# Optimization experiments

Measured on AMD Instinct MI355X. Metric: run time of the kernel, lower is better.

The kernel has to match this reference:

```python
import jax, jax.numpy as jnp
import numpy as np

B, S, HID = 2, 2048, 2048
H, KVH, D = 16, 4, 128
GROUPS = H // KVH  # 4


def apply_rotary(x, cos, sin):
    # x: [B, h, S, D]; cos/sin: [S, D//2]
    xr = x[..., 0::2]
    xi = x[..., 1::2]
    c = cos[None, None, :, :]
    s = sin[None, None, :, :]
    orr = xr * c - xi * s
    oi = xr * s + xi * c
    return jnp.stack([orr, oi], axis=-1).reshape(x.shape)


def setup_inputs() -> dict:
    key = jax.random.key(0)
    k0, k1, k2, k3, k4 = jax.random.split(key, 5)
    x = jax.random.normal(k0, (B, S, HID), dtype=jnp.float32)
    # real RoPE frequencies (llama-style), stored as [S, D//2, 2] = (cos, sin)
    inv_freq = 1.0 / (10000.0 ** (np.arange(0, D, 2, dtype=np.float32) / D))
    t = np.arange(S, dtype=np.float32)
    ang = np.outer(t, inv_freq)  # [S, D//2]
    freqs_cis = jnp.asarray(np.stack([np.cos(ang), np.sin(ang)], axis=-1), dtype=jnp.float32)
    sc = 0.02
    wq = jax.random.normal(k1, (HID, H * D), dtype=jnp.float32) * sc
    wk = jax.random.normal(k2, (HID, KVH * D), dtype=jnp.float32) * sc
    wv = jax.random.normal(k3, (HID, KVH * D), dtype=jnp.float32) * sc
    wo = jax.random.normal(k4, (H * D, HID), dtype=jnp.float32) * sc
    return {"x": x, "freqs_cis": freqs_cis, "wq": wq, "wk": wk, "wv": wv, "wo": wo}


def reference(x, freqs_cis, wq, wk, wv, wo):
    b, s, _ = x.shape
    cos, sin = freqs_cis[..., 0], freqs_cis[..., 1]
    q = (x @ wq).reshape(b, s, H, D).transpose(0, 2, 1, 3)    # [B,H,S,D]
    k = (x @ wk).reshape(b, s, KVH, D).transpose(0, 2, 1, 3)  # [B,KVH,S,D]
    v = (x @ wv).reshape(b, s, KVH, D).transpose(0, 2, 1, 3)
    q = apply_rotary(q, cos, sin)
    k = apply_rotary(k, cos, sin)
    # GQA expand: repeat kv heads into query-head groups
    k = jnp.repeat(k, GROUPS, axis=1)  # [B,H,S,D]
    v = jnp.repeat(v, GROUPS, axis=1)
    scale = 1.0 / jnp.sqrt(jnp.asarray(D, dtype=x.dtype))
    scores = jnp.einsum("bhqd,bhkd->bhqk", q, k) * scale
    causal = jnp.tril(jnp.ones((s, s), dtype=bool))
    scores = jnp.where(causal[None, None], scores, jnp.asarray(-jnp.inf, dtype=scores.dtype))
    attn = jax.nn.softmax(scores, axis=-1)
    out = jnp.einsum("bhqk,bhkd->bhqd", attn, v)
    out = out.transpose(0, 2, 1, 3).reshape(b, s, H * D)
    return out @ wo
```

## Files before the change

### kernel.cpp

```cpp
#include <hip/hip_runtime.h>
#include <hip/hip_bf16.h>

#define B_   2
#define S_   2048
#define HID_ 2048
#define H_   16
#define KVH_ 4
#define D_   128
#define M_   4096
#define NQKV 3072

typedef __attribute__((ext_vector_type(8))) short bf16x8;
typedef __attribute__((ext_vector_type(4))) float f32x4;
typedef __attribute__((ext_vector_type(16))) float f32x16;
typedef const __attribute__((address_space(1))) unsigned int* gas_p;
typedef __attribute__((address_space(3))) unsigned int* las_p;

__device__ __forceinline__ unsigned short f2b(float f) {
    __hip_bfloat16 h = __float2bfloat16(f);
    return *reinterpret_cast<unsigned short*>(&h);
}
__device__ __forceinline__ float b2f(unsigned short u) {
    __hip_bfloat16 h;
    *reinterpret_cast<unsigned short*>(&h) = u;
    return __bfloat162float(h);
}

__global__ __launch_bounds__(256)
void convert_x(const float* __restrict__ x, unsigned short* __restrict__ xb) {
    int i = (blockIdx.x * 256 + threadIdx.x) * 4;
    float4 v = *(const float4*)(x + i);
    ushort4 o;
    o.x = f2b(v.x); o.y = f2b(v.y); o.z = f2b(v.z); o.w = f2b(v.w);
    *(ushort4*)(xb + i) = o;
}

__global__ __launch_bounds__(256)
void convert_w_all(const float* __restrict__ wq, const float* __restrict__ wk,
                   const float* __restrict__ wv, const float* __restrict__ wo,
                   unsigned short* __restrict__ wqkvT,
                   unsigned short* __restrict__ woT) {
    __shared__ float tile[32][33];
    int z = blockIdx.z;
    const float* w; int N, nbase; unsigned short* dst;
    if (z == 0)      { w = wq; N = 2048; nbase = 0;    dst = wqkvT; }
    else if (z == 1) { w = wk; N = 512;  nbase = 2048; dst = wqkvT; }
    else if (z == 2) { w = wv; N = 512;  nbase = 2560; dst = wqkvT; }
    else             { w = wo; N = 2048; nbase = 0;    dst = woT; }
    int n0 = blockIdx.x * 32, k0 = blockIdx.y * 32;
    if (n0 >= N) return;
    int tx = threadIdx.x & 31, ty = threadIdx.x >> 5;
    #pragma unroll
    for (int j = 0; j < 4; j++)
        tile[ty + j*8][tx] = w[(size_t)(k0 + ty + j*8) * N + n0 + tx];
    __syncthreads();
    #pragma unroll
    for (int j = 0; j < 4; j++)
        dst[(size_t)(nbase + n0 + ty + j*8) * 2048 + k0 + tx] = f2b(tile[tx][ty + j*8]);
}

#define BAR    asm volatile("s_barrier" ::: "memory")
#define LG0    do { asm volatile("s_waitcnt lgkmcnt(0)" ::: "memory"); \
                    __builtin_amdgcn_sched_barrier(0); } while (0)
#define GATE6  asm volatile("s_waitcnt vmcnt(6)" ::: "memory")
#define GATE0  asm volatile("s_waitcnt vmcnt(0)" ::: "memory")
#define PHI    __builtin_amdgcn_s_setprio(1)
#define PLO    __builtin_amdgcn_s_setprio(0)

#define STG(srcrow, ldsbase, half, tile) do {                                   \
    _Pragma("unroll")                                                           \
    for (int it_ = 0; it_ < 2; ++it_) {                                         \
      int p_ = w * 128 + it_ * 64 + lane;                                       \
      int r_ = (half) * 128 + (p_ >> 3);                                        \
      int q8_ = ((p_ & 7) ^ ((p_ >> 3) & 7)) * 8;                               \
      __builtin_amdgcn_global_load_lds(                                         \
          (gas_p)((srcrow) + (size_t)r_ * 2048 + (tile) * 64 + q8_),            \
          (las_p)((char*)(ldsbase) + ((half) * 1024 + w * 128 + it_ * 64) * 16),\
          16, 0, 0);                                                            \
    } } while (0)

#define RD_AF(bufi, mi) do {                                                    \
    const unsigned short* Ab_ = &As[bufi][0] + (mi) * 8192 + wr * 4096 + l15 * 64; \
    _Pragma("unroll")                                                           \
    for (int f_ = 0; f_ < 4; ++f_) {                                            \
      af[f_][0] = *(const bf16x8*)(Ab_ + f_ * 1024 + slot0);                    \
      af[f_][1] = *(const bf16x8*)(Ab_ + f_ * 1024 + slot1);                    \
    } } while (0)

#define RD_BF(bufi, ni) do {                                                    \
    const unsigned short* Bb_ = &Bs[bufi][0] + (ni) * 8192 + wc * 2048 + l15 * 64; \
    _Pragma("unroll")                                                           \
    for (int g_ = 0; g_ < 2; ++g_) {                                            \
      bfr[ni][g_][0] = *(const bf16x8*)(Bb_ + g_ * 1024 + slot0);               \
      bfr[ni][g_][1] = *(const bf16x8*)(Bb_ + g_ * 1024 + slot1);               \
    } } while (0)

#define MM(mi, ni) do {                                                         \
    _Pragma("unroll")                                                           \
    for (int f_ = 0; f_ < 4; ++f_)                                              \
      _Pragma("unroll")                                                         \
      for (int g_ = 0; g_ < 2; ++g_) {                                          \
        acc[(mi)*4 + f_][(ni)*2 + g_] = __builtin_amdgcn_mfma_f32_16x16x32_bf16(\
            af[f_][0], bfr[ni][g_][0], acc[(mi)*4 + f_][(ni)*2 + g_], 0, 0, 0); \
        acc[(mi)*4 + f_][(ni)*2 + g_] = __builtin_amdgcn_mfma_f32_16x16x32_bf16(\
            af[f_][1], bfr[ni][g_][1], acc[(mi)*4 + f_][(ni)*2 + g_], 0, 0, 0); \
      } } while (0)

__global__ __launch_bounds__(512)
void gemm8(const unsigned short* __restrict__ A,
           const unsigned short* __restrict__ BT,
           int mode,
           unsigned short* __restrict__ qkvb,
           unsigned short* __restrict__ vTb,
           const float* __restrict__ freqs,
           float* __restrict__ Cf) {
    __shared__ unsigned short As[2][16384];
    __shared__ unsigned short Bs[2][16384];

    int tid  = threadIdx.x;
    int lane = tid & 63, w = tid >> 6;
    int l15  = lane & 15, quad = lane >> 4;
    int wr = w >> 2, wc = w & 3;
    int row0 = blockIdx.y * 256, col0 = blockIdx.x * 256;
    int slot0 = (quad ^ (lane & 7)) * 8;
    int slot1 = slot0 ^ 32;

    const unsigned short* Arow = A  + (size_t)row0 * 2048;
    const unsigned short* Brow = BT + (size_t)col0 * 2048;

    f32x4 acc[8][4];
    #pragma unroll
    for (int i = 0; i < 8; ++i)
        #pragma unroll
        for (int j = 0; j < 4; ++j) acc[i][j] = f32x4{0.f, 0.f, 0.f, 0.f};

    bf16x8 af[4][2];
    bf16x8 bfr[2][2][2];

    STG(Arow, &As[0][0], 0, 0);
    STG(Brow, &Bs[0][0], 0, 0);
    STG(Arow, &As[0][0], 1, 0);
    STG(Brow, &Bs[0][0], 1, 0);
    STG(Arow, &As[1][0], 0, 1);
    STG(Brow, &Bs[1][0], 0, 1);
    STG(Brow, &Bs[1][0], 1, 1);
    GATE6;
    BAR;

    #pragma unroll 1
    for (int i = 0; i < 15; ++i) {
        int t = 2 * i;
        RD_AF(0, 0); RD_BF(0, 0); STG(Arow, &As[1][0], 1, t + 1);
        BAR; LG0; PHI; MM(0, 0); PLO; BAR;
        RD_BF(0, 1); STG(Arow, &As[0][0], 0, t + 2);
        BAR; LG0; PHI; MM(0, 1); PLO; BAR;
        RD_AF(0, 1); STG(Brow, &Bs[0][0], 0, t + 2);
        BAR; LG0; PHI; MM(1, 0); PLO; BAR;
        STG(Brow, &Bs[0][0], 1, t + 2);
        BAR; LG0; PHI; MM(1, 1); PLO; GATE6; BAR;
        RD_AF(1, 0); RD_BF(1, 0); STG(Arow, &As[0][0], 1, t + 2);
        BAR; LG0; PHI; MM(0, 0); PLO; BAR;
        RD_BF(1, 1); STG(Arow, &As[1][0], 0, t + 3);
        BAR; LG0; PHI; MM(0, 1); PLO; BAR;
        RD_AF(1, 1); STG(Brow, &Bs[1][0], 0, t + 3);
        BAR; LG0; PHI; MM(1, 0); PLO; BAR;
        STG(Brow, &Bs[1][0], 1, t + 3);
        BAR; LG0; PHI; MM(1, 1); PLO; GATE6; BAR;
    }
    RD_AF(0, 0); RD_BF(0, 0); STG(Arow, &As[1][0], 1, 31);
    BAR; LG0; PHI; MM(0, 0); PLO; BAR;
    RD_BF(0, 1);
    BAR; LG0; PHI; MM(0, 1); PLO; BAR;
    RD_AF(0, 1);
    BAR; LG0; PHI; MM(1, 0); PLO; BAR;
    BAR; LG0; PHI; MM(1, 1); PLO; GATE0; BAR;
    RD_AF(1, 0); RD_BF(1, 0);
    BAR; LG0; PHI; MM(0, 0); PLO; BAR;
    RD_BF(1, 1);
    BAR; LG0; PHI; MM(0, 1); PLO; BAR;
    RD_AF(1, 1);
    BAR; LG0; PHI; MM(1, 0); PLO; BAR;
    LG0; PHI; MM(1, 1); PLO;

    int q4 = quad * 4;
    if (mode == 0) {
        if (col0 < 2560) {
            #pragma unroll
            for (int mi = 0; mi < 2; ++mi)
            #pragma unroll
            for (int f = 0; f < 4; ++f) {
                int mb = row0 + mi*128 + wr*64 + f*16 + q4;
                #pragma unroll
                for (int ni = 0; ni < 2; ++ni)
                #pragma unroll
                for (int g = 0; g < 2; ++g) {
                    int colb = col0 + ni*128 + wc*32 + g*16 + l15;
                    int dd = (colb & 127) & ~1;
                    bool odd = colb & 1;
                    #pragma unroll
                    for (int rr = 0; rr < 4; ++rr) {
                        int m = mb + rr;
                        int s = m & 2047;
                        float v  = acc[mi*4 + f][ni*2 + g][rr];
                        float pv = __shfl_xor(v, 1);
                        float cs = freqs[s*128 + dd];
                        float sn = freqs[s*128 + dd + 1];
                        float o  = odd ? (pv*sn + v*cs) : (v*cs - pv*sn);
                        qkvb[(size_t)m * NQKV + colb] = f2b(o);
                    }
                }
            }
        } else {
            #pragma unroll
            for (int mi = 0; mi < 2; ++mi)
            #pragma unroll
            for (int f = 0; f < 4; ++f) {
                int mb = row0 + mi*128 + wr*64 + f*16 + q4;
                int s0 = mb & 2047;
                #pragma unroll
                for (int ni = 0; ni < 2; ++ni)
                #pragma unroll
                for (int g = 0; g < 2; ++g) {
                    int colb = col0 + ni*128 + wc*32 + g*16 + l15;
                    int vrow = (row0 >> 11) * 512 + (colb - 2560);
                    ushort4 ov;
                    ov.x = f2b(acc[mi*4 + f][ni*2 + g][0]);
                    ov.y = f2b(acc[mi*4 + f][ni*2 + g][1]);
                    ov.z = f2b(acc[mi*4 + f][ni*2 + g][2]);
                    ov.w = f2b(acc[mi*4 + f][ni*2 + g][3]);
                    *(ushort4*)(vTb + (size_t)vrow * 2048 + s0) = ov;
                }
            }
        }
    } else {
        #pragma unroll
        for (int mi = 0; mi < 2; ++mi)
        #pragma unroll
        for (int f = 0; f < 4; ++f) {
            int mb = row0 + mi*128 + wr*64 + f*16 + q4;
            #pragma unroll
            for (int ni = 0; ni < 2; ++ni)
            #pragma unroll
            for (int g = 0; g < 2; ++g) {
                int colb = col0 + ni*128 + wc*32 + g*16 + l15;
                #pragma unroll
                for (int rr = 0; rr < 4; ++rr)
                    Cf[(size_t)(mb + rr) * 2048 + colb] = acc[mi*4 + f][ni*2 + g][rr];
            }
        }
    }
}

__global__ __launch_bounds__(512)
void attn_mfma(const unsigned short* __restrict__ qkv,
               const unsigned short* __restrict__ vT,
               unsigned short* __restrict__ ao,
               unsigned short* __restrict__ wsP,
               float2* __restrict__ wsML) {
    __shared__ unsigned short Ks[64 * 128];
    __shared__ unsigned short Vt[128 * 64];

    int tid  = threadIdx.x;
    int lane = tid & 63, w = tid >> 6;
    int quad = lane >> 4, l15 = lane & 15;
    int hw = w >> 1, qhalf = w & 1;
    int bx = blockIdx.x, hk = blockIdx.y, b = blockIdx.z;
    int h = hk * 4 + hw;

    int qt, c;
    if (bx < 12)      { qt = 31 - bx / 3;        c = bx % 3; }
    else if (bx < 40) { qt = 27 - (bx - 12) / 2; c = (bx - 12) & 1; }
    else              { qt = 53 - bx;            c = 0; }
    int nt = qt + 1;
    int nch = (qt >= 28) ? 3 : (qt >= 14 ? 2 : 1);
    int kt_begin = c * 14;
    int kt_end = (nt < (c + 1) * 14) ? nt : (c + 1) * 14;
    bool lastc = (c == nch - 1);
    int q0 = qt * 64;
    const float scale = 0.08838834764831845f;

    bf16x8 aq[2][4];
    #pragma unroll
    for (int qf = 0; qf < 2; qf++) {
        const unsigned short* qrow =
            qkv + (size_t)(b*2048 + q0 + qhalf*32 + qf*16 + l15) * NQKV + h*128;
        #pragma unroll
        for (int k4 = 0; k4 < 4; k4++)
            aq[qf][k4] = *(const bf16x8*)(qrow + k4*32 + quad*8);
    }

    int koff[4][4];
    #pragma unroll
    for (int j = 0; j < 4; j++) {
        int row = ((j >> 1) * 32) + ((l15 >> 2) * 8) + ((j & 1) * 4) + (l15 & 3);
        #pragma unroll
        for (int k4 = 0; k4 < 4; k4++) {
            int slot = (k4 * 4 + quad) ^ (row & 15);
            koff[j][k4] = (row * 16 + slot) * 8;
        }
    }
    int vbase0 = (l15 * 8 + (quad ^ (l15 & 7))) * 8;
    int vbase1 = (l15 * 8 + ((4 + quad) ^ (l15 & 7))) * 8;

    const unsigned short* kb0 = qkv + (size_t)(b*2048) * NQKV + 2048 + hk*128;
    const unsigned short* vb0 = vT + (size_t)(b*512 + hk*128) * 2048;

    auto stage_k = [&](int kt) {
        #pragma unroll
        for (int it = 0; it < 2; it++) {
            int s = w * 128 + it * 64 + lane;
            int r = s >> 4, qp = s & 15;
            int q = qp ^ (r & 15);
            __builtin_amdgcn_global_load_lds(
                (gas_p)(kb0 + (size_t)(kt*64 + r) * NQKV + q * 8),
                (las_p)((char*)&Ks[0] + (w * 128 + it * 64) * 16),
                16, 0, 0);
        }
    };
    auto stage_v = [&](int kt) {
        #pragma unroll
        for (int it = 0; it < 2; it++) {
            int s = w * 128 + it * 64 + lane;
            int r = s >> 3, qp = s & 7;
            int q = qp ^ (r & 7);
            __builtin_amdgcn_global_load_lds(
                (gas_p)(vb0 + (size_t)r * 2048 + kt*64 + q * 8),
                (las_p)((char*)&Vt[0] + (w * 128 + it * 64) * 16),
                16, 0, 0);
        }
    };

    f32x4 o_acc[2][8];
    const f32x4 zf = {0.f, 0.f, 0.f, 0.f};
    #pragma unroll
    for (int qf = 0; qf < 2; qf++)
        #pragma unroll
        for (int jn = 0; jn < 8; jn++) o_acc[qf][jn] = zf;
    float m_i[2] = {-1e30f, -1e30f}, l_i[2] = {0.f, 0.f};
    int qglob[2] = {q0 + qhalf*32 + l15, q0 + qhalf*32 + 16 + l15};

    stage_k(kt_begin);
    for (int kt = kt_begin; kt < kt_end; kt++) {
        __syncthreads();
        stage_v(kt);

        f32x4 s_acc[2][4];
        #pragma unroll
        for (int j = 0; j < 4; j++) {
            s_acc[0][j] = zf; s_acc[1][j] = zf;
            #pragma unroll
            for (int k4 = 0; k4 < 4; k4++) {
                bf16x8 ak = *(const bf16x8*)&Ks[koff[j][k4]];
                s_acc[0][j] = __builtin_amdgcn_mfma_f32_16x16x32_bf16(ak, aq[0][k4], s_acc[0][j], 0, 0, 0);
                s_acc[1][j] = __builtin_amdgcn_mfma_f32_16x16x32_bf16(ak, aq[1][k4], s_acc[1][j], 0, 0, 0);
            }
        }

        bf16x8 pp[2][2];
        #pragma unroll
        for (int qf = 0; qf < 2; qf++) {
            float sv[4][4];
            #pragma unroll
            for (int j = 0; j < 4; j++)
                #pragma unroll
                for (int r = 0; r < 4; r++)
                    sv[j][r] = s_acc[qf][j][r] * scale;
            if (kt == qt) {
                #pragma unroll
                for (int j = 0; j < 4; j++)
                    #pragma unroll
                    for (int r = 0; r < 4; r++) {
                        int sloc = ((j >> 1) * 32) + quad*8 + ((j & 1) * 4) + r;
                        if (kt*64 + sloc > qglob[qf]) sv[j][r] = -1e30f;
                    }
            }
            float mx = sv[0][0];
            #pragma unroll
            for (int j = 0; j < 4; j++)
                #pragma unroll
                for (int r = 0; r < 4; r++) mx = fmaxf(mx, sv[j][r]);
            mx = fmaxf(mx, __shfl_xor(mx, 16));
            mx = fmaxf(mx, __shfl_xor(mx, 32));
            float mnew = fmaxf(m_i[qf], mx);
            float alpha = __expf(m_i[qf] - mnew);
            float rs = 0.f;
            float p[4][4];
            #pragma unroll
            for (int j = 0; j < 4; j++)
                #pragma unroll
                for (int r = 0; r < 4; r++) {
                    p[j][r] = __expf(sv[j][r] - mnew);
                    rs += p[j][r];
                }
            l_i[qf] = l_i[qf] * alpha + rs;
            m_i[qf] = mnew;
            #pragma unroll
            for (int jn = 0; jn < 8; jn++)
                #pragma unroll
                for (int r = 0; r < 4; r++) o_acc[qf][jn][r] *= alpha;
            #pragma unroll
            for (int r = 0; r < 4; r++) {
                pp[qf][0][r]     = (short)f2b(p[0][r]);
                pp[qf][0][r + 4] = (short)f2b(p[1][r]);
                pp[qf][1][r]     = (short)f2b(p[2][r]);
                pp[qf][1][r + 4] = (short)f2b(p[3][r]);
            }
        }

        __syncthreads();
        if (kt + 1 < kt_end) stage_k(kt + 1);

        #pragma unroll
        for (int jn = 0; jn < 8; jn++) {
            bf16x8 av0 = *(const bf16x8*)&Vt[jn*1024 + vbase0];
            bf16x8 av1 = *(const bf16x8*)&Vt[jn*1024 + vbase1];
            o_acc[0][jn] = __builtin_amdgcn_mfma_f32_16x16x32_bf16(av0, pp[0][0], o_acc[0][jn], 0, 0, 0);
            o_acc[0][jn] = __builtin_amdgcn_mfma_f32_16x16x32_bf16(av1, pp[0][1], o_acc[0][jn], 0, 0, 0);
            o_acc[1][jn] = __builtin_amdgcn_mfma_f32_16x16x32_bf16(av0, pp[1][0], o_acc[1][jn], 0, 0, 0);
            o_acc[1][jn] = __builtin_amdgcn_mfma_f32_16x16x32_bf16(av1, pp[1][1], o_acc[1][jn], 0, 0, 0);
        }
    }

    int pi = 0, mi = 0;
    if (qt >= 14) {
        if (qt < 28) { mi = (qt - 14) * 2 + c;       pi = qt - 14; }
        else         { mi = 28 + (qt - 28) * 3 + c;  pi = 14 + (qt - 28) * 2 + c; }
    }
    #pragma unroll
    for (int qf = 0; qf < 2; qf++) {
        float lt = l_i[qf];
        lt += __shfl_xor(lt, 16);
        lt += __shfl_xor(lt, 32);
        float inv = 1.f / lt;
        int q_local = qhalf * 32 + qf * 16 + l15;
        unsigned short* dst;
        if (lastc)
            dst = ao + (size_t)(b*2048 + q0 + q_local) * 2048 + h*128;
        else
            dst = wsP + (size_t)(((pi * 8 + hk * 2 + b) * 4 + hw) * 64 + q_local) * 128;
        #pragma unroll
        for (int jn = 0; jn < 8; jn++) {
            ushort4 ov;
            ov.x = f2b(o_acc[qf][jn][0] * inv);
            ov.y = f2b(o_acc[qf][jn][1] * inv);
            ov.z = f2b(o_acc[qf][jn][2] * inv);
            ov.w = f2b(o_acc[qf][jn][3] * inv);
            *(ushort4*)(dst + jn*16 + quad*4) = ov;
        }
        if (qt >= 14 && quad == 0)
            wsML[(mi * 8 + hk * 2 + b) * 256 + hw * 64 + q_local]
                = make_float2(m_i[qf], lt);
    }
}

__global__ __launch_bounds__(256)
void merge_kernel(unsigned short* __restrict__ ao,
                  const unsigned short* __restrict__ wsP,
                  const float2* __restrict__ wsML) {
    int t = blockIdx.x * 256 + threadIdx.x;
    int d = (t & 15) * 8;
    int h = (t >> 4) & 15;
    int rest = t >> 8;
    int q_off = rest % 1152;
    int b = rest / 1152;
    int q = 896 + q_off;
    int qt = q >> 6, q_local = q & 63;
    int hk = h >> 2, hw = h & 3;
    int nch = (qt >= 28) ? 3 : 2;

    float mv[3], lv[3];
    for (int cc = 0; cc < nch; cc++) {
        int mi = (qt < 28) ? (qt - 14) * 2 + cc : 28 + (qt - 28) * 3 + cc;
        float2 ml = wsML[(mi * 8 + hk * 2 + b) * 256 + hw * 64 + q_local];
        mv[cc] = ml.x; lv[cc] = ml.y;
    }
    float M = mv[0];
    for (int cc = 1; cc < nch; cc++) M = fmaxf(M, mv[cc]);
    float f[3], S = 0.f;
    for (int cc = 0; cc < nch; cc++) { f[cc] = __expf(mv[cc] - M) * lv[cc]; S += f[cc]; }
    float inv = 1.f / S;

    unsigned short* arow = ao + (size_t)(b*2048 + q) * 2048 + h*128 + d;
    float outv[8];
    {
        ushort4 a0 = *(ushort4*)arow, a1 = *(ushort4*)(arow + 4);
        float fl = f[nch-1];
        outv[0] = fl*b2f(a0.x); outv[1] = fl*b2f(a0.y);
        outv[2] = fl*b2f(a0.z); outv[3] = fl*b2f(a0.w);
        outv[4] = fl*b2f(a1.x); outv[5] = fl*b2f(a1.y);
        outv[6] = fl*b2f(a1.z); outv[7] = fl*b2f(a1.w);
    }
    for (int cc = 0; cc < nch - 1; cc++) {
        int pi = (qt < 28) ? (qt - 14) : 14 + (qt - 28) * 2 + cc;
        const unsigned short* prow =
            wsP + (size_t)(((pi * 8 + hk * 2 + b) * 4 + hw) * 64 + q_local) * 128 + d;
        ushort4 p0 = *(const ushort4*)prow, p1 = *(const ushort4*)(prow + 4);
        float fc = f[cc];
        outv[0] += fc*b2f(p0.x); outv[1] += fc*b2f(p0.y);
        outv[2] += fc*b2f(p0.z); outv[3] += fc*b2f(p0.w);
        outv[4] += fc*b2f(p1.x); outv[5] += fc*b2f(p1.y);
        outv[6] += fc*b2f(p1.z); outv[7] += fc*b2f(p1.w);
    }
    ushort4 o0, o1;
    o0.x = f2b(outv[0]*inv); o0.y = f2b(outv[1]*inv);
    o0.z = f2b(outv[2]*inv); o0.w = f2b(outv[3]*inv);
    o1.x = f2b(outv[4]*inv); o1.y = f2b(outv[5]*inv);
    o1.z = f2b(outv[6]*inv); o1.w = f2b(outv[7]*inv);
    *(ushort4*)arow = o0;
    *(ushort4*)(arow + 4) = o1;
}

extern "C" void kernel_launch(void* const* d_in, const int* in_sizes, int n_in,
                              void* d_out, int out_size, void* d_ws, size_t ws_size,
                              hipStream_t stream) {
    const float* x     = (const float*)d_in[0];
    const float* freqs = (const float*)d_in[1];
    const float* wq    = (const float*)d_in[2];
    const float* wk    = (const float*)d_in[3];
    const float* wv    = (const float*)d_in[4];
    const float* wo    = (const float*)d_in[5];
    float* out = (float*)d_out;

    char* ws = (char*)d_ws;
    unsigned short* xbf    = (unsigned short*)(ws);
    unsigned short* aobuf  = (unsigned short*)(ws);
    unsigned short* wqkvT  = (unsigned short*)(ws + (16u<<20));
    unsigned short* woT    = (unsigned short*)(ws + (28u<<20));
    unsigned short* qkvbuf = (unsigned short*)(ws + (36u<<20));
    unsigned short* vTbuf  = (unsigned short*)(ws + (60u<<20));
    unsigned short* wsP  = (unsigned short*)(ws + (16u<<20));
    float2*         wsML = (float2*)(ws + (16u<<20) + 176u*65536u);

    dim3 blk(256);
    convert_x<<<8192, blk, 0, stream>>>(x, xbf);
    convert_w_all<<<dim3(64, 64, 4), blk, 0, stream>>>(wq, wk, wv, wo, wqkvT, woT);
    gemm8<<<dim3(NQKV/256, M_/256), dim3(512), 0, stream>>>(
        xbf, wqkvT, 0, qkvbuf, vTbuf, freqs, nullptr);
    attn_mfma<<<dim3(54, 4, 2), dim3(512), 0, stream>>>(qkvbuf, vTbuf, aobuf, wsP, wsML);
    merge_kernel<<<2304, blk, 0, stream>>>(aobuf, wsP, wsML);
    gemm8<<<dim3(2048/256, M_/256), dim3(512), 0, stream>>>(
        aobuf, woT, 1, nullptr, nullptr, nullptr, out);
}
```

Baseline: 348.5 us.

## Add dedicated 256x128-tile output GEMM and XCD-aware block remapping

Splits the output projection into its own kernel, gemm8o, which uses 256x128 tiles. On a 4096x2048 problem that launches 256 blocks instead of 128, filling more of the GPU's compute units, at the cost of lower per-block reuse of the A operand. Both GEMMs now remap block IDs so that consecutive IDs, which land on different XCDs, map to nearby tiles on the same XCD, aiming for better L2 locality. The QKV kernel also drops its runtime mode branch.

```diff
diff --git a/kernel.cpp b/kernel.cpp
--- a/kernel.cpp
+++ b/kernel.cpp
@@ -109,11 +109,9 @@
 __global__ __launch_bounds__(512)
 void gemm8(const unsigned short* __restrict__ A,
            const unsigned short* __restrict__ BT,
-           int mode,
            unsigned short* __restrict__ qkvb,
            unsigned short* __restrict__ vTb,
-           const float* __restrict__ freqs,
-           float* __restrict__ Cf) {
+           const float* __restrict__ freqs) {
     __shared__ unsigned short As[2][16384];
     __shared__ unsigned short Bs[2][16384];
 
@@ -121,7 +119,10 @@
     int lane = tid & 63, w = tid >> 6;
     int l15  = lane & 15, quad = lane >> 4;
     int wr = w >> 2, wc = w & 3;
-    int row0 = blockIdx.y * 256, col0 = blockIdx.x * 256;
+    int bid = blockIdx.y * 12 + blockIdx.x;
+    int s_  = (bid & 7) * 24 + (bid >> 3);
+    int by  = s_ / 12, bx = s_ % 12;
+    int row0 = by * 256, col0 = bx * 256;
     int slot0 = (quad ^ (lane & 7)) * 8;
     int slot1 = slot0 ^ 32;
 
@@ -183,54 +184,31 @@
     LG0; PHI; MM(1, 1); PLO;
 
     int q4 = quad * 4;
-    if (mode == 0) {
-        if (col0 < 2560) {
-            #pragma unroll
-            for (int mi = 0; mi < 2; ++mi)
-            #pragma unroll
-            for (int f = 0; f < 4; ++f) {
-                int mb = row0 + mi*128 + wr*64 + f*16 + q4;
+    if (col0 < 2560) {
+        #pragma unroll
+        for (int mi = 0; mi < 2; ++mi)
+        #pragma unroll
+        for (int f = 0; f < 4; ++f) {
+            int mb = row0 + mi*128 + wr*64 + f*16 + q4;
+            #pragma unroll
+            for (int ni = 0; ni < 2; ++ni)
+            #pragma unroll
+            for (int g = 0; g < 2; ++g) {
+                int colb = col0 + ni*128 + wc*32 + g*16 + l15;
+                int dd = (colb & 127) & ~1;
+                bool odd = colb & 1;
                 #pragma unroll
-                for (int ni = 0; ni < 2; ++ni)
-                #pragma unroll
-                for (int g = 0; g < 2; ++g) {
-                    int colb = col0 + ni*128 + wc*32 + g*16 + l15;
-                    int dd = (colb & 127) & ~1;
-                    bool odd = colb & 1;
-                    #pragma unroll
-                    for (int rr = 0; rr < 4; ++rr) {
-                        int m = mb + rr;
-                        int s = m & 2047;
-                        float v  = acc[mi*4 + f][ni*2 + g][rr];
-                        float pv = __shfl_xor(v, 1);
-                        float cs = freqs[s*128 + dd];
-                        float sn = freqs[s*128 + dd + 1];
-                        float o  = odd ? (pv*sn + v*cs) : (v*cs - pv*sn);
-                        qkvb[(size_t)m * NQKV + colb] = f2b(o);
-                    }
+                for (int rr = 0; rr < 4; ++rr) {
+                    int m = mb + rr;
+                    int s = m & 2047;
+                    float v  = acc[mi*4 + f][ni*2 + g][rr];
+                    float pv = __shfl_xor(v, 1);
+                    float cs = freqs[s*128 + dd];
+                    float sn = freqs[s*128 + dd + 1];
+                    float o  = odd ? (pv*sn + v*cs) : (v*cs - pv*sn);
+                    qkvb[(size_t)m * NQKV + colb] = f2b(o);
                 }
             }
-        } else {
-            #pragma unroll
-            for (int mi = 0; mi < 2; ++mi)
-            #pragma unroll
-            for (int f = 0; f < 4; ++f) {
-                int mb = row0 + mi*128 + wr*64 + f*16 + q4;
-                int s0 = mb & 2047;
-                #pragma unroll
-                for (int ni = 0; ni < 2; ++ni)
-                #pragma unroll
-                for (int g = 0; g < 2; ++g) {
-                    int colb = col0 + ni*128 + wc*32 + g*16 + l15;
-                    int vrow = (row0 >> 11) * 512 + (colb - 2560);
-                    ushort4 ov;
-                    ov.x = f2b(acc[mi*4 + f][ni*2 + g][0]);
-                    ov.y = f2b(acc[mi*4 + f][ni*2 + g][1]);
-                    ov.z = f2b(acc[mi*4 + f][ni*2 + g][2]);
-                    ov.w = f2b(acc[mi*4 + f][ni*2 + g][3]);
-                    *(ushort4*)(vTb + (size_t)vrow * 2048 + s0) = ov;
-                }
-            }
         }
     } else {
         #pragma unroll
@@ -238,15 +216,131 @@
         #pragma unroll
         for (int f = 0; f < 4; ++f) {
             int mb = row0 + mi*128 + wr*64 + f*16 + q4;
+            int s0 = mb & 2047;
             #pragma unroll
             for (int ni = 0; ni < 2; ++ni)
             #pragma unroll
             for (int g = 0; g < 2; ++g) {
                 int colb = col0 + ni*128 + wc*32 + g*16 + l15;
-                #pragma unroll
-                for (int rr = 0; rr < 4; ++rr)
-                    Cf[(size_t)(mb + rr) * 2048 + colb] = acc[mi*4 + f][ni*2 + g][rr];
+                int vrow = (row0 >> 11) * 512 + (colb - 2560);
+                ushort4 ov;
+                ov.x = f2b(acc[mi*4 + f][ni*2 + g][0]);
+                ov.y = f2b(acc[mi*4 + f][ni*2 + g][1]);
+                ov.z = f2b(acc[mi*4 + f][ni*2 + g][2]);
+                ov.w = f2b(acc[mi*4 + f][ni*2 + g][3]);
+                *(ushort4*)(vTb + (size_t)vrow * 2048 + s0) = ov;
             }
+        }
+    }
+}
+
+#define RDA(bufi) do {                                                          \
+    const unsigned short* Ab_ = &As[bufi][0] + wr * 4096 + l15 * 64;            \
+    _Pragma("unroll")                                                           \
+    for (int f_ = 0; f_ < 4; ++f_) {                                            \
+      af[f_][0] = *(const bf16x8*)(Ab_ + f_ * 1024 + slot0);                    \
+      af[f_][1] = *(const bf16x8*)(Ab_ + f_ * 1024 + slot1);                    \
+    } } while (0)
+
+#define RDB(bufi, g) do {                                                       \
+    const unsigned short* Bb_ = &Bs[bufi][0] + wc * 4096 + l15 * 64;            \
+    bfr[g][0] = *(const bf16x8*)(Bb_ + (g) * 1024 + slot0);                     \
+    bfr[g][1] = *(const bf16x8*)(Bb_ + (g) * 1024 + slot1);                     \
+    } while (0)
+
+#define MM8(mi, ni) do {                                                        \
+    _Pragma("unroll")                                                           \
+    for (int f_ = 2*(mi); f_ < 2*(mi)+2; ++f_)                                  \
+      _Pragma("unroll")                                                         \
+      for (int g_ = 2*(ni); g_ < 2*(ni)+2; ++g_) {                              \
+        acc[f_][g_] = __builtin_amdgcn_mfma_f32_16x16x32_bf16(                  \
+            af[f_][0], bfr[g_][0], acc[f_][g_], 0, 0, 0);                       \
+        acc[f_][g_] = __builtin_amdgcn_mfma_f32_16x16x32_bf16(                  \
+            af[f_][1], bfr[g_][1], acc[f_][g_], 0, 0, 0);                       \
+      } } while (0)
+
+__global__ __launch_bounds__(512)
+void gemm8o(const unsigned short* __restrict__ A,
+            const unsigned short* __restrict__ BT,
+            float* __restrict__ Cf) {
+    __shared__ unsigned short As[2][16384];
+    __shared__ unsigned short Bs[2][8192];
+
+    int tid  = threadIdx.x;
+    int lane = tid & 63, w = tid >> 6;
+    int l15  = lane & 15, quad = lane >> 4;
+    int wr = w >> 1, wc = w & 1;
+    int bid = blockIdx.y * 16 + blockIdx.x;
+    int s_  = (bid & 7) * 32 + (bid >> 3);
+    int by  = s_ >> 4, bx = s_ & 15;
+    int row0 = by * 256, col0 = bx * 128;
+    int slot0 = (quad ^ (lane & 7)) * 8;
+    int slot1 = slot0 ^ 32;
+
+    const unsigned short* Arow = A  + (size_t)row0 * 2048;
+    const unsigned short* Brow = BT + (size_t)col0 * 2048;
+
+    f32x4 acc[4][4];
+    #pragma unroll
+    for (int i = 0; i < 4; ++i)
+        #pragma unroll
+        for (int j = 0; j < 4; ++j) acc[i][j] = f32x4{0.f, 0.f, 0.f, 0.f};
+
+    bf16x8 af[4][2];
+    bf16x8 bfr[4][2];
+
+    STG(Arow, &As[0][0], 0, 0);
+    STG(Arow, &As[0][0], 1, 0);
+    STG(Brow, &Bs[0][0], 0, 0);
+    STG(Arow, &As[1][0], 0, 1);
+    STG(Arow, &As[1][0], 1, 1);
+    STG(Brow, &Bs[1][0], 0, 1);
+    GATE6;
+    BAR;
+
+    #pragma unroll 1
+    for (int i = 0; i < 15; ++i) {
+        int t = 2 * i;
+        RDA(0); RDB(0, 0); RDB(0, 1);
+        BAR; LG0; PHI; MM8(0, 0); PLO; BAR;
+        RDB(0, 2); RDB(0, 3); STG(Arow, &As[0][0], 0, t + 2);
+        BAR; LG0; PHI; MM8(0, 1); PLO; BAR;
+        STG(Arow, &As[0][0], 1, t + 2);
+        BAR; LG0; PHI; MM8(1, 0); PLO; BAR;
+        STG(Brow, &Bs[0][0], 0, t + 2);
+        BAR; LG0; PHI; MM8(1, 1); PLO; GATE6; BAR;
+        RDA(1); RDB(1, 0); RDB(1, 1);
+        BAR; LG0; PHI; MM8(0, 0); PLO; BAR;
+        RDB(1, 2); RDB(1, 3); STG(Arow, &As[1][0], 0, t + 3);
+        BAR; LG0; PHI; MM8(0, 1); PLO; BAR;
+        STG(Arow, &As[1][0], 1, t + 3);
+        BAR; LG0; PHI; MM8(1, 0); PLO; BAR;
+        STG(Brow, &Bs[1][0], 0, t + 3);
+        BAR; LG0; PHI; MM8(1, 1); PLO; GATE6; BAR;
+    }
+    RDA(0); RDB(0, 0); RDB(0, 1);
+    BAR; LG0; PHI; MM8(0, 0); PLO; BAR;
+    RDB(0, 2); RDB(0, 3);
+    BAR; LG0; PHI; MM8(0, 1); PLO; BAR;
+    BAR; LG0; PHI; MM8(1, 0); PLO; BAR;
+    BAR; LG0; PHI; MM8(1, 1); PLO; GATE0; BAR;
+    RDA(1); RDB(1, 0); RDB(1, 1);
+    BAR; LG0; PHI; MM8(0, 0); PLO; BAR;
+    RDB(1, 2); RDB(1, 3);
+    BAR; LG0; PHI; MM8(0, 1); PLO; BAR;
+    BAR; LG0; PHI; MM8(1, 0); PLO; BAR;
+    LG0; PHI; MM8(1, 1); PLO;
+
+    int q4 = quad * 4;
+    #pragma unroll
+    for (int f = 0; f < 4; ++f) {
+        int mb = row0 + wr*64 + f*16 + q4;
+        #pragma unroll
+        for (int g = 0; g < 4; ++g) {
+            int colb = col0 + wc*64 + g*16 + l15;
+            #pragma unroll
+            for (int rr = 0; rr < 4; ++rr)
+                Cf[(size_t)(mb + rr) * 2048 + colb] = acc[f][g][rr];
         }
     }
 }
@@ -535,9 +629,8 @@
     convert_x<<<8192, blk, 0, stream>>>(x, xbf);
     convert_w_all<<<dim3(64, 64, 4), blk, 0, stream>>>(wq, wk, wv, wo, wqkvT, woT);
     gemm8<<<dim3(NQKV/256, M_/256), dim3(512), 0, stream>>>(
-        xbf, wqkvT, 0, qkvbuf, vTbuf, freqs, nullptr);
+        xbf, wqkvT, qkvbuf, vTbuf, freqs);
     attn_mfma<<<dim3(54, 4, 2), dim3(512), 0, stream>>>(qkvbuf, vTbuf, aobuf, wsP, wsML);
     merge_kernel<<<2304, blk, 0, stream>>>(aobuf, wsP, wsML);
-    gemm8<<<dim3(2048/256, M_/256), dim3(512), 0, stream>>>(
-        aobuf, woT, 1, nullptr, nullptr, nullptr, out);
-}
+    gemm8o<<<dim3(2048/128, M_/256), dim3(512), 0, stream>>>(aobuf, woT, out);
+}
```

Result: faster. 318.2 us (-8.7%).

## Software-pipeline GEMM LDS reads with MFMA, add XCD block swizzle, smaller output GEMM

Applied to the files above, without the earlier changes.

Restructures the QKV GEMM main loop to double-buffer the register fragments, so LDS reads for the next quadrant are issued while MFMAs run on the current one. This removes the per-step lgkmcnt(0) waits and half the barriers. Block indices are remapped so neighbouring tiles land on the same XCD for better L2 reuse. The output projection moves to a new 128x128-tile, 256-thread kernel that launches more blocks (512 instead of 128) to fill the CUs, at the cost of reloading more operand data per FLOP. The implicit LDS waits now rely on the compiler inserting the correct lgkmcnt.

```diff
diff --git a/kernel.cpp b/kernel.cpp
--- a/kernel.cpp
+++ b/kernel.cpp
@@ -12,7 +12,6 @@
 
 typedef __attribute__((ext_vector_type(8))) short bf16x8;
 typedef __attribute__((ext_vector_type(4))) float f32x4;
-typedef __attribute__((ext_vector_type(16))) float f32x16;
 typedef const __attribute__((address_space(1))) unsigned int* gas_p;
 typedef __attribute__((address_space(3))) unsigned int* las_p;
 
@@ -60,10 +59,10 @@
 }
 
 #define BAR    asm volatile("s_barrier" ::: "memory")
-#define LG0    do { asm volatile("s_waitcnt lgkmcnt(0)" ::: "memory"); \
-                    __builtin_amdgcn_sched_barrier(0); } while (0)
+#define GATE2  asm volatile("s_waitcnt vmcnt(2)" ::: "memory")
+#define GATE4  asm volatile("s_waitcnt vmcnt(4)" ::: "memory")
 #define GATE6  asm volatile("s_waitcnt vmcnt(6)" ::: "memory")
-#define GATE0  asm volatile("s_waitcnt vmcnt(0)" ::: "memory")
+#define GATE8  asm volatile("s_waitcnt vmcnt(8)" ::: "memory")
 #define PHI    __builtin_amdgcn_s_setprio(1)
 #define PLO    __builtin_amdgcn_s_setprio(0)
 
@@ -79,41 +78,39 @@
           16, 0, 0);                                                            \
     } } while (0)
 
-#define RD_AF(bufi, mi) do {                                                    \
-    const unsigned short* Ab_ = &As[bufi][0] + (mi) * 8192 + wr * 4096 + l15 * 64; \
+#define RDA2(dst, bufi, mi) do {                                                \
+    const unsigned short* Ab_ = &As[bufi][0] + (mi)*8192 + wr*4096 + l15*64;    \
     _Pragma("unroll")                                                           \
     for (int f_ = 0; f_ < 4; ++f_) {                                            \
-      af[f_][0] = *(const bf16x8*)(Ab_ + f_ * 1024 + slot0);                    \
-      af[f_][1] = *(const bf16x8*)(Ab_ + f_ * 1024 + slot1);                    \
+      dst[f_][0] = *(const bf16x8*)(Ab_ + f_*1024 + slot0);                     \
+      dst[f_][1] = *(const bf16x8*)(Ab_ + f_*1024 + slot1);                     \
     } } while (0)
 
-#define RD_BF(bufi, ni) do {                                                    \
-    const unsigned short* Bb_ = &Bs[bufi][0] + (ni) * 8192 + wc * 2048 + l15 * 64; \
+#define RDB2(dst, bufi, ni) do {                                                \
+    const unsigned short* Bb_ = &Bs[bufi][0] + (ni)*8192 + wc*2048 + l15*64;    \
     _Pragma("unroll")                                                           \
     for (int g_ = 0; g_ < 2; ++g_) {                                            \
-      bfr[ni][g_][0] = *(const bf16x8*)(Bb_ + g_ * 1024 + slot0);               \
-      bfr[ni][g_][1] = *(const bf16x8*)(Bb_ + g_ * 1024 + slot1);               \
+      dst[g_][0] = *(const bf16x8*)(Bb_ + g_*1024 + slot0);                     \
+      dst[g_][1] = *(const bf16x8*)(Bb_ + g_*1024 + slot1);                     \
     } } while (0)
 
-#define MM(mi, ni) do {                                                         \
+#define MMQ(ra, rb, mi, ni) do {                                                \
     _Pragma("unroll")                                                           \
     for (int f_ = 0; f_ < 4; ++f_)                                              \
       _Pragma("unroll")                                                         \
       for (int g_ = 0; g_ < 2; ++g_) {                                          \
-        acc[(mi)*4 + f_][(ni)*2 + g_] = __builtin_amdgcn_mfma_f32_16x16x32_bf16(\
-            af[f_][0], bfr[ni][g_][0], acc[(mi)*4 + f_][(ni)*2 + g_], 0, 0, 0); \
-        acc[(mi)*4 + f_][(ni)*2 + g_] = __builtin_amdgcn_mfma_f32_16x16x32_bf16(\
-            af[f_][1], bfr[ni][g_][1], acc[(mi)*4 + f_][(ni)*2 + g_], 0, 0, 0); \
+        acc[(mi)*4+f_][(ni)*2+g_] = __builtin_amdgcn_mfma_f32_16x16x32_bf16(    \
+            ra[f_][0], rb[g_][0], acc[(mi)*4+f_][(ni)*2+g_], 0, 0, 0);          \
+        acc[(mi)*4+f_][(ni)*2+g_] = __builtin_amdgcn_mfma_f32_16x16x32_bf16(    \
+            ra[f_][1], rb[g_][1], acc[(mi)*4+f_][(ni)*2+g_], 0, 0, 0);          \
       } } while (0)
 
 __global__ __launch_bounds__(512)
 void gemm8(const unsigned short* __restrict__ A,
            const unsigned short* __restrict__ BT,
-           int mode,
            unsigned short* __restrict__ qkvb,
            unsigned short* __restrict__ vTb,
-           const float* __restrict__ freqs,
-           float* __restrict__ Cf) {
+           const float* __restrict__ freqs) {
     __shared__ unsigned short As[2][16384];
     __shared__ unsigned short Bs[2][16384];
 
@@ -121,7 +118,10 @@
     int lane = tid & 63, w = tid >> 6;
     int l15  = lane & 15, quad = lane >> 4;
     int wr = w >> 2, wc = w & 3;
-    int row0 = blockIdx.y * 256, col0 = blockIdx.x * 256;
+    int bid = blockIdx.y * 12 + blockIdx.x;
+    int s_  = (bid & 7) * 24 + (bid >> 3);
+    int by  = s_ / 12, bx = s_ % 12;
+    int row0 = by * 256, col0 = bx * 256;
     int slot0 = (quad ^ (lane & 7)) * 8;
     int slot1 = slot0 ^ 32;
 
@@ -134,119 +134,241 @@
         #pragma unroll
         for (int j = 0; j < 4; ++j) acc[i][j] = f32x4{0.f, 0.f, 0.f, 0.f};
 
-    bf16x8 af[4][2];
-    bf16x8 bfr[2][2][2];
-
+    bf16x8 ra0[4][2], ra1[4][2];
+    bf16x8 rb0[2][2], rb1[2][2];
+
+    STG(Brow, &Bs[0][0], 0, 0);
     STG(Arow, &As[0][0], 0, 0);
-    STG(Brow, &Bs[0][0], 0, 0);
     STG(Arow, &As[0][0], 1, 0);
     STG(Brow, &Bs[0][0], 1, 0);
+    STG(Brow, &Bs[1][0], 0, 1);
     STG(Arow, &As[1][0], 0, 1);
-    STG(Brow, &Bs[1][0], 0, 1);
+    STG(Arow, &As[1][0], 1, 1);
     STG(Brow, &Bs[1][0], 1, 1);
+    GATE8;
+    BAR;
+    RDB2(rb0, 0, 0);
+    RDA2(ra0, 0, 0);
+
+    #pragma unroll 1
+    for (int i = 0; i < 16; ++i) {
+        int t  = 2 * i;
+        int t2 = (t + 2 > 31) ? 31 : t + 2;
+        int t3 = (t + 3 > 31) ? 31 : t + 3;
+        RDA2(ra1, 0, 1);
+        PHI; MMQ(ra0, rb0, 0, 0); PLO;
+        STG(Brow, &Bs[0][0], 0, t2);
+        BAR;
+        RDB2(rb1, 0, 1);
+        PHI; MMQ(ra1, rb0, 1, 0); PLO;
+        STG(Arow, &As[0][0], 0, t2);
+        GATE8; BAR;
+        RDB2(rb0, 1, 0);
+        PHI; MMQ(ra0, rb1, 0, 1); PLO;
+        STG(Arow, &As[0][0], 1, t2);
+        BAR;
+        RDA2(ra0, 1, 0);
+        PHI; MMQ(ra1, rb1, 1, 1); PLO;
+        STG(Brow, &Bs[0][0], 1, t2);
+        GATE8; BAR;
+        RDA2(ra1, 1, 1);
+        PHI; MMQ(ra0, rb0, 0, 0); PLO;
+        STG(Brow, &Bs[1][0], 0, t3);
+        BAR;
+        RDB2(rb1, 1, 1);
+        PHI; MMQ(ra1, rb0, 1, 0); PLO;
+        STG(Arow, &As[1][0], 0, t3);
+        GATE8; BAR;
+        RDB2(rb0, 0, 0);
+        PHI; MMQ(ra0, rb1, 0, 1); PLO;
+        STG(Arow, &As[1][0], 1, t3);
+        BAR;
+        RDA2(ra0, 0, 0);
+        PHI; MMQ(ra1, rb1, 1, 1); PLO;
+        STG(Brow, &Bs[1][0], 1, t3);
+        GATE8; BAR;
+    }
+
+    int q4 = quad * 4;
+    if (col0 < 2560) {
+        #pragma unroll
+        for (int mi = 0; mi < 2; ++mi)
+        #pragma unroll
+        for (int f = 0; f < 4; ++f) {
+            int mb = row0 + mi*128 + wr*64 + f*16 + q4;
+            #pragma unroll
+            for (int ni = 0; ni < 2; ++ni)
+            #pragma unroll
+            for (int g = 0; g < 2; ++g) {
+                int colb = col0 + ni*128 + wc*32 + g*16 + l15;
+                int dd = (colb & 127) & ~1;
+                bool odd = colb & 1;
+                #pragma unroll
+                for (int rr = 0; rr < 4; ++rr) {
+                    int m = mb + rr;
+                    int s = m & 2047;
+                    float v  = acc[mi*4 + f][ni*2 + g][rr];
+                    float pv = __shfl_xor(v, 1);
+                    float cs = freqs[s*128 + dd];
+                    float sn = freqs[s*128 + dd + 1];
+                    float o  = odd ? (pv*sn + v*cs) : (v*cs - pv*sn);
+                    qkvb[(size_t)m * NQKV + colb] = f2b(o);
+                }
+            }
+        }
+    } else {
+        #pragma unroll
+        for (int mi = 0; mi < 2; ++mi)
+        #pragma unroll
+        for (int f = 0; f < 4; ++f) {
+            int mb = row0 + mi*128 + wr*64 + f*16 + q4;
+            int s0 = mb & 2047;
+            #pragma unroll
+            for (int ni = 0; ni < 2; ++ni)
+            #pragma unroll
+            for (int g = 0; g < 2; ++g) {
+                int colb = col0 + ni*128 + wc*32 + g*16 + l15;
+                int vrow = (row0 >> 11) * 512 + (colb - 2560);
+                ushort4 ov;
+                ov.x = f2b(acc[mi*4 + f][ni*2 + g][0]);
+                ov.y = f2b(acc[mi*4 + f][ni*2 + g][1]);
+                ov.z = f2b(acc[mi*4 + f][ni*2 + g][2]);
+                ov.w = f2b(acc[mi*4 + f][ni*2 + g][3]);
+                *(ushort4*)(vTb + (size_t)vrow * 2048 + s0) = ov;
+            }
+        }
+    }
+}
+
+#define STGO(srcrow, ldsbase, unit, tile) do {                                  \
+    _Pragma("unroll")                                                           \
+    for (int it_ = 0; it_ < 2; ++it_) {                                         \
+      int p_ = w * 128 + it_ * 64 + lane;                                       \
+      int r_ = (unit) * 64 + (p_ >> 3);                                         \
+      int q8_ = ((p_ & 7) ^ ((p_ >> 3) & 7)) * 8;                               \
+      __builtin_amdgcn_global_load_lds(                                         \
+          (gas_p)((srcrow) + (size_t)r_ * 2048 + (tile) * 64 + q8_),            \
+          (las_p)((char*)(ldsbase) + ((unit) * 512 + w * 128 + it_ * 64) * 16), \
+          16, 0, 0);                                                            \
+    } } while (0)
+
+#define RDA3(dst, bufi, pp) do {                                                \
+    const unsigned short* Ab_ = &As[bufi][0] + wr*4096 + l15*64;                \
+    _Pragma("unroll")                                                           \
+    for (int f_ = 0; f_ < 2; ++f_) {                                            \
+      dst[f_][0] = *(const bf16x8*)(Ab_ + ((pp)*2+f_)*1024 + slot0);            \
+      dst[f_][1] = *(const bf16x8*)(Ab_ + ((pp)*2+f_)*1024 + slot1);            \
+    } } while (0)
+
+#define RDB3(dst, bufi, pp) do {                                                \
+    const unsigned short* Bb_ = &Bs[bufi][0] + wc*4096 + l15*64;                \
+    _Pragma("unroll")                                                           \
+    for (int g_ = 0; g_ < 2; ++g_) {                                            \
+      dst[g_][0] = *(const bf16x8*)(Bb_ + ((pp)*2+g_)*1024 + slot0);            \
+      dst[g_][1] = *(const bf16x8*)(Bb_ + ((pp)*2+g_)*1024 + slot1);            \
+    } } while (0)
+
+#define MMQ3(ra, rb, mi, ni) do {                                               \
+    _Pragma("unroll")                                                           \
+    for (int f_ = 0; f_ < 2; ++f_)                                              \
+      _Pragma("unroll")                                                         \
+      for (int g_ = 0; g_ < 2; ++g_) {                                          \
+        acc[(mi)*2+f_][(ni)*2+g_] = __builtin_amdgcn_mfma_f32_16x16x32_bf16(    \
+            ra[f_][0], rb[g_][0], acc[(mi)*2+f_][(ni)*2+g_], 0, 0, 0);          \
+        acc[(mi)*2+f_][(ni)*2+g_] = __builtin_amdgcn_mfma_f32_16x16x32_bf16(    \
+            ra[f_][1], rb[g_][1], acc[(mi)*2+f_][(ni)*2+g_], 0, 0, 0);          \
+      } } while (0)
+
+__global__ __launch_bounds__(256)
+void gemm8o(const unsigned short* __restrict__ A,
+            const unsigned short* __restrict__ BT,
+            float* __restrict__ Cf) {
+    __shared__ unsigned short As[2][8192];
+    __shared__ unsigned short Bs[2][8192];
+
+    int tid  = threadIdx.x;
+    int lane = tid & 63, w = tid >> 6;
+    int l15  = lane & 15, quad = lane >> 4;
+    int wr = w >> 1, wc = w & 1;
+    int bid = blockIdx.y * 16 + blockIdx.x;
+    int s_  = (bid & 7) * 64 + (bid >> 3);
+    int by  = s_ >> 4, bx = s_ & 15;
+    int row0 = by * 128, col0 = bx * 128;
+    int slot0 = (quad ^ (lane & 7)) * 8;
+    int slot1 = slot0 ^ 32;
+
+    const unsigned short* Arow = A  + (size_t)row0 * 2048;
+    const unsigned short* Brow = BT + (size_t)col0 * 2048;
+
+    f32x4 acc[4][4];
+    #pragma unroll
+    for (int i = 0; i < 4; ++i)
+        #pragma unroll
+        for (int j = 0; j < 4; ++j) acc[i][j] = f32x4{0.f, 0.f, 0.f, 0.f};
+
+    bf16x8 a0[2][2], a1[2][2], b0[2][2], b1[2][2];
+
+    STGO(Arow, &As[0][0], 0, 0);
+    STGO(Arow, &As[0][0], 1, 0);
+    STGO(Brow, &Bs[0][0], 0, 0);
+    STGO(Brow, &Bs[0][0], 1, 0);
+    STGO(Arow, &As[1][0], 0, 1);
+    STGO(Brow, &Bs[1][0], 0, 1);
+    STGO(Brow, &Bs[1][0], 1, 1);
     GATE6;
     BAR;
+    RDB3(b0, 0, 0);
+    RDA3(a0, 0, 0);
 
     #pragma unroll 1
-    for (int i = 0; i < 15; ++i) {
-        int t = 2 * i;
-        RD_AF(0, 0); RD_BF(0, 0); STG(Arow, &As[1][0], 1, t + 1);
-        BAR; LG0; PHI; MM(0, 0); PLO; BAR;
-        RD_BF(0, 1); STG(Arow, &As[0][0], 0, t + 2);
-        BAR; LG0; PHI; MM(0, 1); PLO; BAR;
-        RD_AF(0, 1); STG(Brow, &Bs[0][0], 0, t + 2);
-        BAR; LG0; PHI; MM(1, 0); PLO; BAR;
-        STG(Brow, &Bs[0][0], 1, t + 2);
-        BAR; LG0; PHI; MM(1, 1); PLO; GATE6; BAR;
-        RD_AF(1, 0); RD_BF(1, 0); STG(Arow, &As[0][0], 1, t + 2);
-        BAR; LG0; PHI; MM(0, 0); PLO; BAR;
-        RD_BF(1, 1); STG(Arow, &As[1][0], 0, t + 3);
-        BAR; LG0; PHI; MM(0, 1); PLO; BAR;
-        RD_AF(1, 1); STG(Brow, &Bs[1][0], 0, t + 3);
-        BAR; LG0; PHI; MM(1, 0); PLO; BAR;
-        STG(Brow, &Bs[1][0], 1, t + 3);
-        BAR; LG0; PHI; MM(1, 1); PLO; GATE6; BAR;
-    }
-    RD_AF(0, 0); RD_BF(0, 0); STG(Arow, &As[1][0], 1, 31);
-    BAR; LG0; PHI; MM(0, 0); PLO; BAR;
-    RD_BF(0, 1);
-    BAR; LG0; PHI; MM(0, 1); PLO; BAR;
-    RD_AF(0, 1);
-    BAR; LG0; PHI; MM(1, 0); PLO; BAR;
-    BAR; LG0; PHI; MM(1, 1); PLO; GATE0; BAR;
-    RD_AF(1, 0); RD_BF(1, 0);
-    BAR; LG0; PHI; MM(0, 0); PLO; BAR;
-    RD_BF(1, 1);
-    BAR; LG0; PHI; MM(0, 1); PLO; BAR;
-    RD_AF(1, 1);
-    BAR; LG0; PHI; MM(1, 0); PLO; BAR;
-    LG0; PHI; MM(1, 1); PLO;
+    for (int i = 0; i < 16; ++i) {
+        int t  = 2 * i;
+        int t2 = (t + 2 > 31) ? 31 : t + 2;
+        int t3 = (t + 3 > 31) ? 31 : t + 3;
+        RDA3(a1, 0, 1);
+        PHI; MMQ3(a0, b0, 0, 0); PLO;
+        STGO(Arow, &As[1][0], 1, t + 1);
+        BAR;
+        RDB3(b1, 0, 1);
+        PHI; MMQ3(a1, b0, 1, 0); PLO;
+        STGO(Arow, &As[0][0], 0, t2);
+        GATE2; BAR;
+        RDB3(b0, 1, 0);
+        PHI; MMQ3(a0, b1, 0, 1); PLO;
+        STGO(Arow, &As[0][0], 1, t2);
+        BAR;
+        RDA3(a0, 1, 0);
+        PHI; MMQ3(a1, b1, 1, 1); PLO;
+        STGO(Brow, &Bs[0][0], 0, t2);
+        GATE4; BAR;
+        RDA3(a1, 1, 1);
+        PHI; MMQ3(a0, b0, 0, 0); PLO;
+        STGO(Brow, &Bs[0][0], 1, t2);
+        BAR;
+        RDB3(b1, 1, 1);
+        PHI; MMQ3(a1, b0, 1, 0); PLO;
+        STGO(Arow, &As[1][0], 0, t3);
+        GATE2; BAR;
+        RDB3(b0, 0, 0);
+        PHI; MMQ3(a0, b1, 0, 1); PLO;
+        STGO(Brow, &Bs[1][0], 0, t3);
+        BAR;
+        RDA3(a0, 0, 0);
+        PHI; MMQ3(a1, b1, 1, 1); PLO;
+        STGO(Brow, &Bs[1][0], 1, t3);
+        GATE4; BAR;
+    }
 
     int q4 = quad * 4;
-    if (mode == 0) {
-        if (col0 < 2560) {
-            #pragma unroll
-            for (int mi = 0; mi < 2; ++mi)
-            #pragma unroll
-            for (int f = 0; f < 4; ++f) {
-                int mb = row0 + mi*128 + wr*64 + f*16 + q4;
-                #pragma unroll
-                for (int ni = 0; ni < 2; ++ni)
-                #pragma unroll
-                for (int g = 0; g < 2; ++g) {
-                    int colb = col0 + ni*128 + wc*32 + g*16 + l15;
-                    int dd = (colb & 127) & ~1;
-                    bool odd = colb & 1;
-                    #pragma unroll
-                    for (int rr = 0; rr < 4; ++rr) {
-                        int m = mb + rr;
-                        int s = m & 2047;
-                        float v  = acc[mi*4 + f][ni*2 + g][rr];
-                        float pv = __shfl_xor(v, 1);
-                        float cs = freqs[s*128 + dd];
-                        float sn = freqs[s*128 + dd + 1];
-                        float o  = odd ? (pv*sn + v*cs) : (v*cs - pv*sn);
-                        qkvb[(size_t)m * NQKV + colb] = f2b(o);
-                    }
-                }
-            }
-        } else {
-            #pragma unroll
-            for (int mi = 0; mi < 2; ++mi)
-            #pragma unroll
-            for (int f = 0; f < 4; ++f) {
-                int mb = row0 + mi*128 + wr*64 + f*16 + q4;
-                int s0 = mb & 2047;
-                #pragma unroll
-                for (int ni = 0; ni < 2; ++ni)
-                #pragma unroll
-                for (int g = 0; g < 2; ++g) {
-                    int colb = col0 + ni*128 + wc*32 + g*16 + l15;
-                    int vrow = (row0 >> 11) * 512 + (colb - 2560);
-                    ushort4 ov;
-                    ov.x = f2b(acc[mi*4 + f][ni*2 + g][0]);
-                    ov.y = f2b(acc[mi*4 + f][ni*2 + g][1]);
-                    ov.z = f2b(acc[mi*4 + f][ni*2 + g][2]);
-                    ov.w = f2b(acc[mi*4 + f][ni*2 + g][3]);
-                    *(ushort4*)(vTb + (size_t)vrow * 2048 + s0) = ov;
-                }
-            }
-        }
-    } else {
-        #pragma unroll
-        for (int mi = 0; mi < 2; ++mi)
-        #pragma unroll
-        for (int f = 0; f < 4; ++f) {
-            int mb = row0 + mi*128 + wr*64 + f*16 + q4;
-            #pragma unroll
-            for (int ni = 0; ni < 2; ++ni)
-            #pragma unroll
-            for (int g = 0; g < 2; ++g) {
-                int colb = col0 + ni*128 + wc*32 + g*16 + l15;
-                #pragma unroll
-                for (int rr = 0; rr < 4; ++rr)
-                    Cf[(size_t)(mb + rr) * 2048 + colb] = acc[mi*4 + f][ni*2 + g][rr];
-            }
+    #pragma unroll
+    for (int f = 0; f < 4; ++f) {
+        int mb = row0 + wr*64 + f*16 + q4;
+        #pragma unroll
+        for (int g = 0; g < 4; ++g) {
+            int colb = col0 + wc*64 + g*16 + l15;
+            #pragma unroll
+            for (int rr = 0; rr < 4; ++rr)
+                Cf[(size_t)(mb + rr) * 2048 + colb] = acc[f][g][rr];
         }
     }
 }
@@ -535,9 +657,8 @@
     convert_x<<<8192, blk, 0, stream>>>(x, xbf);
     convert_w_all<<<dim3(64, 64, 4), blk, 0, stream>>>(wq, wk, wv, wo, wqkvT, woT);
     gemm8<<<dim3(NQKV/256, M_/256), dim3(512), 0, stream>>>(
-        xbf, wqkvT, 0, qkvbuf, vTbuf, freqs, nullptr);
+        xbf, wqkvT, qkvbuf, vTbuf, freqs);
     attn_mfma<<<dim3(54, 4, 2), dim3(512), 0, stream>>>(qkvbuf, vTbuf, aobuf, wsP, wsML);
     merge_kernel<<<2304, blk, 0, stream>>>(aobuf, wsP, wsML);
-    gemm8<<<dim3(2048/256, M_/256), dim3(512), 0, stream>>>(
-        aobuf, woT, 1, nullptr, nullptr, nullptr, out);
-}
+    gemm8o<<<dim3(2048/128, M_/128), blk, 0, stream>>>(aobuf, woT, out);
+}
```

Measured after the change: 328.7 us. -5.7%, faster.
